# Kernel tuning notes

Measured on AMD Instinct MI355X. Metric: run time of the kernel, lower is better.

Reference implementation:

```python
import jax, jax.numpy as jnp
import numpy as np

B, S, H, C = 16, 4096, 1024, 64

def setup_inputs() -> dict:
    key = jax.random.key(0)
    k1, k2 = jax.random.split(key)
    hidden = jax.random.normal(k1, (B, S, H), dtype=jnp.float32)
    querys = jax.random.normal(k2, (C, H), dtype=jnp.float32)
    return {"hidden": hidden, "querys": querys}

def reference(hidden, querys):
    # scores: [B, C, S] = einsum over hidden_size
    scores = jnp.einsum('bsh,ch->bcs', hidden, querys)
    # softmax over the sequence axis
    factor = jax.nn.softmax(scores, axis=2)
    # pooled: [B, C, H]
    result = jnp.einsum('bcs,bsh->bch', factor, hidden)
    # flatten to [B, C*H]
    return result.reshape(-1, querys.shape[0] * querys.shape[1])
```

## Files before the change

### kernel.cpp

```cpp
#include <hip/hip_runtime.h>
#include <math.h>

#define BB 16
#define SS 4096
#define HH 1024
#define CC 64

typedef __attribute__((ext_vector_type(4))) float f32x4;
typedef __attribute__((ext_vector_type(8))) short s16x8;

__device__ __forceinline__ ushort f2bf(float x) {
    union { float f; unsigned u; } un; un.f = x;
    unsigned r = (un.u + 0x7FFFu + ((un.u >> 16) & 1u)) >> 16;
    return (ushort)r;
}
__device__ __forceinline__ float bf2f(ushort h) {
    union { unsigned u; float f; } un; un.u = ((unsigned)h) << 16; return un.f;
}

__global__ __launch_bounds__(256) void prep_querys_kernel(
    const float* __restrict__ q, ushort* __restrict__ qhi, ushort* __restrict__ qlo)
{
    const int i4 = blockIdx.x * 256 + threadIdx.x;
    const float4 v = ((const float4*)q)[i4];
    ushort4 h, l;
    h.x = f2bf(v.x); l.x = f2bf(v.x - bf2f(h.x));
    h.y = f2bf(v.y); l.y = f2bf(v.y - bf2f(h.y));
    h.z = f2bf(v.z); l.z = f2bf(v.z - bf2f(h.z));
    h.w = f2bf(v.w); l.w = f2bf(v.w - bf2f(h.w));
    ((ushort4*)qhi)[i4] = h;
    ((ushort4*)qlo)[i4] = l;
}

__global__ __launch_bounds__(256) void scores_kernel(
    const float* __restrict__ hidden, const ushort* __restrict__ qhi,
    const ushort* __restrict__ qlo, float* __restrict__ scores)
{
    __shared__ __align__(16) ushort Ahi[128][40];
    __shared__ __align__(16) ushort Alo[128][40];
    __shared__ __align__(16) ushort Bhi[64][40];
    __shared__ __align__(16) ushort Blo[64][40];

    const int b  = blockIdx.y;
    const int s0 = blockIdx.x * 128;
    const int t  = threadIdx.x;
    const int w    = t >> 6;
    const int lane = t & 63;
    const int col  = lane & 15;
    const int quad = lane >> 4;
    const int lr = t >> 3;
    const int lc = t & 7;

    f32x4 acc[2][4];
#pragma unroll
    for (int i = 0; i < 2; ++i)
#pragma unroll
        for (int j = 0; j < 4; ++j) acc[i][j] = (f32x4){0.f, 0.f, 0.f, 0.f};

    const float* hbase = hidden + ((size_t)b * SS + s0) * HH;

    float4 hv[4];
    ushort4 qh[2], ql[2];
#pragma unroll
    for (int p = 0; p < 4; ++p)
        hv[p] = *(const float4*)&hbase[(size_t)(lr + 32 * p) * HH + lc * 4];
#pragma unroll
    for (int p = 0; p < 2; ++p) {
        qh[p] = ((const ushort4*)qhi)[(lr + 32 * p) * 256 + lc];
        ql[p] = ((const ushort4*)qlo)[(lr + 32 * p) * 256 + lc];
    }

    for (int k0 = 0; k0 < HH; k0 += 32) {
        __syncthreads();
#pragma unroll
        for (int p = 0; p < 4; ++p) {
            const int r = lr + 32 * p;
            ushort4 h, l;
            h.x = f2bf(hv[p].x); l.x = f2bf(hv[p].x - bf2f(h.x));
            h.y = f2bf(hv[p].y); l.y = f2bf(hv[p].y - bf2f(h.y));
            h.z = f2bf(hv[p].z); l.z = f2bf(hv[p].z - bf2f(h.z));
            h.w = f2bf(hv[p].w); l.w = f2bf(hv[p].w - bf2f(h.w));
            *(ushort4*)&Ahi[r][lc * 4] = h;
            *(ushort4*)&Alo[r][lc * 4] = l;
        }
#pragma unroll
        for (int p = 0; p < 2; ++p) {
            *(ushort4*)&Bhi[lr + 32 * p][lc * 4] = qh[p];
            *(ushort4*)&Blo[lr + 32 * p][lc * 4] = ql[p];
        }
        __syncthreads();

        if (k0 + 32 < HH) {
            const int kn = k0 + 32;
#pragma unroll
            for (int p = 0; p < 4; ++p)
                hv[p] = *(const float4*)&hbase[(size_t)(lr + 32 * p) * HH + kn + lc * 4];
#pragma unroll
            for (int p = 0; p < 2; ++p) {
                qh[p] = ((const ushort4*)qhi)[(lr + 32 * p) * 256 + kn / 4 + lc];
                ql[p] = ((const ushort4*)qlo)[(lr + 32 * p) * 256 + kn / 4 + lc];
            }
        }

        s16x8 ah[2], al[2], bh[4], bl[4];
#pragma unroll
        for (int mt = 0; mt < 2; ++mt) {
            const int r = w * 32 + mt * 16 + col;
            ah[mt] = *(const s16x8*)&Ahi[r][quad * 8];
            al[mt] = *(const s16x8*)&Alo[r][quad * 8];
        }
#pragma unroll
        for (int nt = 0; nt < 4; ++nt) {
            const int r = nt * 16 + col;
            bh[nt] = *(const s16x8*)&Bhi[r][quad * 8];
            bl[nt] = *(const s16x8*)&Blo[r][quad * 8];
        }
#pragma unroll
        for (int mt = 0; mt < 2; ++mt)
#pragma unroll
            for (int nt = 0; nt < 4; ++nt) {
                acc[mt][nt] = __builtin_amdgcn_mfma_f32_16x16x32_bf16(ah[mt], bh[nt], acc[mt][nt], 0, 0, 0);
                acc[mt][nt] = __builtin_amdgcn_mfma_f32_16x16x32_bf16(ah[mt], bl[nt], acc[mt][nt], 0, 0, 0);
                acc[mt][nt] = __builtin_amdgcn_mfma_f32_16x16x32_bf16(al[mt], bh[nt], acc[mt][nt], 0, 0, 0);
            }
    }

#pragma unroll
    for (int mt = 0; mt < 2; ++mt)
#pragma unroll
        for (int nt = 0; nt < 4; ++nt) {
            const int c = nt * 16 + col;
            const int s = s0 + w * 32 + mt * 16 + quad * 4;
            *(f32x4*)&scores[((size_t)(b * CC + c)) * SS + s] = acc[mt][nt];
        }
}

__global__ __launch_bounds__(256) void softmax_kernel(
    const float* __restrict__ scores, ushort* __restrict__ factor)
{
    const float* p = scores + (size_t)blockIdx.x * SS;
    ushort* f = factor + (size_t)blockIdx.x * SS;
    const int t = threadIdx.x;
    float4 v[4];
    float m = -3.0e38f;
#pragma unroll
    for (int i = 0; i < 4; ++i) {
        v[i] = *(const float4*)&p[t * 4 + i * 1024];
        m = fmaxf(m, fmaxf(fmaxf(v[i].x, v[i].y), fmaxf(v[i].z, v[i].w)));
    }
#pragma unroll
    for (int off = 1; off < 64; off <<= 1) m = fmaxf(m, __shfl_xor(m, off));
    __shared__ float redm[4];
    __shared__ float reds[4];
    const int wave = t >> 6, lane = t & 63;
    if (lane == 0) redm[wave] = m;
    __syncthreads();
    m = fmaxf(fmaxf(redm[0], redm[1]), fmaxf(redm[2], redm[3]));

    float sum = 0.0f;
#pragma unroll
    for (int i = 0; i < 4; ++i) {
        v[i].x = __expf(v[i].x - m); v[i].y = __expf(v[i].y - m);
        v[i].z = __expf(v[i].z - m); v[i].w = __expf(v[i].w - m);
        sum += (v[i].x + v[i].y) + (v[i].z + v[i].w);
    }
#pragma unroll
    for (int off = 1; off < 64; off <<= 1) sum += __shfl_xor(sum, off);
    if (lane == 0) reds[wave] = sum;
    __syncthreads();
    sum = (reds[0] + reds[1]) + (reds[2] + reds[3]);
    const float inv = 1.0f / sum;
#pragma unroll
    for (int i = 0; i < 4; ++i) {
        ushort4 o;
        o.x = f2bf(v[i].x * inv); o.y = f2bf(v[i].y * inv);
        o.z = f2bf(v[i].z * inv); o.w = f2bf(v[i].w * inv);
        ((ushort4*)f)[t + i * 256] = o;
    }
}

__global__ __launch_bounds__(256) void pool_kernel(
    const float* __restrict__ hidden, const ushort* __restrict__ factor,
    float* __restrict__ parts)
{
    __shared__ __align__(16) ushort Ht[64][72];

    const int b  = blockIdx.y;
    const int h0 = blockIdx.x * 64;
    const int ks = blockIdx.z;
    const int sbeg = ks * (SS / 4);
    const int t = threadIdx.x;
    const int w = t >> 6, lane = t & 63, col = lane & 15, quad = lane >> 4;
    const int hc = t & 15;
    const int sq = t >> 4;

    f32x4 acc[4];
#pragma unroll
    for (int j = 0; j < 4; ++j) acc[j] = (f32x4){0.f, 0.f, 0.f, 0.f};

    const float* hbase = hidden + (size_t)b * SS * HH + h0;
    const ushort* fbase = factor + (size_t)(b * CC + w * 16 + col) * SS + sbeg;

    float v[16];
#pragma unroll
    for (int pp = 0; pp < 2; ++pp)
#pragma unroll
        for (int mm = 0; mm < 4; ++mm)
#pragma unroll
            for (int e = 0; e < 2; ++e)
                v[pp * 8 + mm * 2 + e] =
                    hbase[(size_t)(sbeg + 2 * (sq + 16 * pp) + e) * HH + hc + 16 * mm];

    for (int sc = 0; sc < SS / 4; sc += 64) {
        __syncthreads();
#pragma unroll
        for (int pp = 0; pp < 2; ++pp)
#pragma unroll
            for (int mm = 0; mm < 4; ++mm) {
                unsigned pack = (unsigned)f2bf(v[pp * 8 + mm * 2 + 0]) |
                                ((unsigned)f2bf(v[pp * 8 + mm * 2 + 1]) << 16);
                ((unsigned*)Ht)[(hc + 16 * mm) * 36 + (sq + 16 * pp)] = pack;
            }
        __syncthreads();

        const s16x8 fa0 = *(const s16x8*)&fbase[sc + quad * 8];
        const s16x8 fa1 = *(const s16x8*)&fbase[sc + 32 + quad * 8];

        if (sc + 64 < SS / 4) {
#pragma unroll
            for (int pp = 0; pp < 2; ++pp)
#pragma unroll
                for (int mm = 0; mm < 4; ++mm)
#pragma unroll
                    for (int e = 0; e < 2; ++e)
                        v[pp * 8 + mm * 2 + e] =
                            hbase[(size_t)(sbeg + sc + 64 + 2 * (sq + 16 * pp) + e) * HH + hc + 16 * mm];
        }

#pragma unroll
        for (int ksp = 0; ksp < 2; ++ksp) {
            const s16x8 fa = ksp ? fa1 : fa0;
#pragma unroll
            for (int nt = 0; nt < 4; ++nt) {
                const s16x8 hb = *(const s16x8*)&Ht[nt * 16 + col][ksp * 32 + quad * 8];
                acc[nt] = __builtin_amdgcn_mfma_f32_16x16x32_bf16(fa, hb, acc[nt], 0, 0, 0);
            }
        }
    }

    float* dst = parts + (size_t)ks * (BB * CC * HH) + (size_t)b * (CC * HH);
#pragma unroll
    for (int nt = 0; nt < 4; ++nt) {
        const int h = h0 + nt * 16 + col;
#pragma unroll
        for (int r = 0; r < 4; ++r) {
            const int c = w * 16 + quad * 4 + r;
            dst[(size_t)c * HH + h] = acc[nt][r];
        }
    }
}

__global__ __launch_bounds__(256) void reduce4_kernel(
    const float* __restrict__ parts, float* __restrict__ out)
{
    const int i = blockIdx.x * 256 + threadIdx.x;
    const float4* p = (const float4*)parts;
    const float4 a = p[i];
    const float4 b = p[i + 262144];
    const float4 c = p[i + 524288];
    const float4 d = p[i + 786432];
    float4 r;
    r.x = (a.x + b.x) + (c.x + d.x);
    r.y = (a.y + b.y) + (c.y + d.y);
    r.z = (a.z + b.z) + (c.z + d.z);
    r.w = (a.w + b.w) + (c.w + d.w);
    ((float4*)out)[i] = r;
}

extern "C" void kernel_launch(void* const* d_in, const int* in_sizes, int n_in,
                              void* d_out, int out_size, void* d_ws, size_t ws_size,
                              hipStream_t stream)
{
    const float* hidden = (const float*)d_in[0];
    const float* querys = (const float*)d_in[1];
    float* out = (float*)d_out;

    float*  scores = (float*)d_ws;
    float*  parts  = (float*)d_ws;
    ushort* factor = (ushort*)((char*)d_ws + (16u << 20));
    ushort* qhi    = (ushort*)((char*)d_ws + (24u << 20));
    ushort* qlo    = qhi + CC * HH;

    prep_querys_kernel<<<dim3(CC * HH / 1024), 256, 0, stream>>>(querys, qhi, qlo);
    scores_kernel<<<dim3(SS / 128, BB), 256, 0, stream>>>(hidden, qhi, qlo, scores);
    softmax_kernel<<<dim3(BB * CC), 256, 0, stream>>>(scores, factor);
    pool_kernel<<<dim3(HH / 64, BB, 4), 256, 0, stream>>>(hidden, factor, parts);
    reduce4_kernel<<<dim3(1024), 256, 0, stream>>>(parts, out);
}
```

Before: 455.8 us.

## Cache bf16 hidden from scores pass and drop LDS staging in both GEMMs

The scores kernel now loads hidden directly into MFMA register fragments without LDS or barriers, converting with a vectorized hi/lo split. It also writes the bf16-high copy of hidden to workspace. The pool kernel then reads that bf16 copy, half the bytes of fp32, gathering column fragments straight from global memory instead of transposing through LDS. The trade-offs are an extra 128MB write in the scores pass, strided 2-byte gathers in pool, and a rounding mode change (round-half-up rather than round-to-nearest-even).

```diff
diff --git a/kernel.cpp b/kernel.cpp
--- a/kernel.cpp
+++ b/kernel.cpp
@@ -8,6 +8,7 @@
 
 typedef __attribute__((ext_vector_type(4))) float f32x4;
 typedef __attribute__((ext_vector_type(8))) short s16x8;
+typedef __attribute__((ext_vector_type(4))) unsigned int u32x4;
 
 __device__ __forceinline__ ushort f2bf(float x) {
     union { float f; unsigned u; } un; un.f = x;
@@ -16,6 +17,27 @@
 }
 __device__ __forceinline__ float bf2f(ushort h) {
     union { unsigned u; float f; } un; un.u = ((unsigned)h) << 16; return un.f;
+}
+
+__device__ __forceinline__ unsigned hipack(unsigned v1, unsigned v0) {
+    return __builtin_amdgcn_perm(v1, v0, 0x07060302u);
+}
+
+__device__ __forceinline__ void cvt8(f32x4 f0, f32x4 f1, s16x8& hi, s16x8& lo) {
+    u32x4 u0 = __builtin_bit_cast(u32x4, f0);
+    u32x4 u1 = __builtin_bit_cast(u32x4, f1);
+    u32x4 b0 = u0 + 0x8000u;
+    u32x4 b1 = u1 + 0x8000u;
+    f32x4 m0 = __builtin_bit_cast(f32x4, b0 & 0xFFFF0000u);
+    f32x4 m1 = __builtin_bit_cast(f32x4, b1 & 0xFFFF0000u);
+    u32x4 r0 = __builtin_bit_cast(u32x4, f0 - m0);
+    u32x4 r1 = __builtin_bit_cast(u32x4, f1 - m1);
+    u32x4 h = { hipack(b0.y, b0.x), hipack(b0.w, b0.z),
+                hipack(b1.y, b1.x), hipack(b1.w, b1.z) };
+    u32x4 l = { hipack(r0.y, r0.x), hipack(r0.w, r0.z),
+                hipack(r1.y, r1.x), hipack(r1.w, r1.z) };
+    hi = __builtin_bit_cast(s16x8, h);
+    lo = __builtin_bit_cast(s16x8, l);
 }
 
 __global__ __launch_bounds__(256) void prep_querys_kernel(
@@ -34,22 +56,22 @@
 
 __global__ __launch_bounds__(256) void scores_kernel(
     const float* __restrict__ hidden, const ushort* __restrict__ qhi,
-    const ushort* __restrict__ qlo, float* __restrict__ scores)
-{
-    __shared__ __align__(16) ushort Ahi[128][40];
-    __shared__ __align__(16) ushort Alo[128][40];
-    __shared__ __align__(16) ushort Bhi[64][40];
-    __shared__ __align__(16) ushort Blo[64][40];
-
+    const ushort* __restrict__ qlo, float* __restrict__ scores,
+    ushort* __restrict__ hid_hi)
+{
     const int b  = blockIdx.y;
     const int s0 = blockIdx.x * 128;
     const int t  = threadIdx.x;
-    const int w    = t >> 6;
-    const int lane = t & 63;
-    const int col  = lane & 15;
-    const int quad = lane >> 4;
-    const int lr = t >> 3;
-    const int lc = t & 7;
+    const int w = t >> 6, lane = t & 63, col = lane & 15, quad = lane >> 4;
+
+    const int r0 = s0 + w * 32 + col;
+    const int r1 = r0 + 16;
+    const float* a0p = hidden + ((size_t)b * SS + r0) * HH + quad * 8;
+    const float* a1p = hidden + ((size_t)b * SS + r1) * HH + quad * 8;
+    ushort* h0p = hid_hi + ((size_t)b * SS + r0) * HH + quad * 8;
+    ushort* h1p = hid_hi + ((size_t)b * SS + r1) * HH + quad * 8;
+    const ushort* qbh = qhi + (size_t)col * HH + quad * 8;
+    const ushort* qbl = qlo + (size_t)col * HH + quad * 8;
 
     f32x4 acc[2][4];
 #pragma unroll
@@ -57,73 +79,39 @@
 #pragma unroll
         for (int j = 0; j < 4; ++j) acc[i][j] = (f32x4){0.f, 0.f, 0.f, 0.f};
 
-    const float* hbase = hidden + ((size_t)b * SS + s0) * HH;
-
-    float4 hv[4];
-    ushort4 qh[2], ql[2];
-#pragma unroll
-    for (int p = 0; p < 4; ++p)
-        hv[p] = *(const float4*)&hbase[(size_t)(lr + 32 * p) * HH + lc * 4];
-#pragma unroll
-    for (int p = 0; p < 2; ++p) {
-        qh[p] = ((const ushort4*)qhi)[(lr + 32 * p) * 256 + lc];
-        ql[p] = ((const ushort4*)qlo)[(lr + 32 * p) * 256 + lc];
-    }
-
-    for (int k0 = 0; k0 < HH; k0 += 32) {
-        __syncthreads();
-#pragma unroll
-        for (int p = 0; p < 4; ++p) {
-            const int r = lr + 32 * p;
-            ushort4 h, l;
-            h.x = f2bf(hv[p].x); l.x = f2bf(hv[p].x - bf2f(h.x));
-            h.y = f2bf(hv[p].y); l.y = f2bf(hv[p].y - bf2f(h.y));
-            h.z = f2bf(hv[p].z); l.z = f2bf(hv[p].z - bf2f(h.z));
-            h.w = f2bf(hv[p].w); l.w = f2bf(hv[p].w - bf2f(h.w));
-            *(ushort4*)&Ahi[r][lc * 4] = h;
-            *(ushort4*)&Alo[r][lc * 4] = l;
-        }
-#pragma unroll
-        for (int p = 0; p < 2; ++p) {
-            *(ushort4*)&Bhi[lr + 32 * p][lc * 4] = qh[p];
-            *(ushort4*)&Blo[lr + 32 * p][lc * 4] = ql[p];
-        }
-        __syncthreads();
-
-        if (k0 + 32 < HH) {
-            const int kn = k0 + 32;
-#pragma unroll
-            for (int p = 0; p < 4; ++p)
-                hv[p] = *(const float4*)&hbase[(size_t)(lr + 32 * p) * HH + kn + lc * 4];
-#pragma unroll
-            for (int p = 0; p < 2; ++p) {
-                qh[p] = ((const ushort4*)qhi)[(lr + 32 * p) * 256 + kn / 4 + lc];
-                ql[p] = ((const ushort4*)qlo)[(lr + 32 * p) * 256 + kn / 4 + lc];
-            }
-        }
-
-        s16x8 ah[2], al[2], bh[4], bl[4];
-#pragma unroll
-        for (int mt = 0; mt < 2; ++mt) {
-            const int r = w * 32 + mt * 16 + col;
-            ah[mt] = *(const s16x8*)&Ahi[r][quad * 8];
-            al[mt] = *(const s16x8*)&Alo[r][quad * 8];
-        }
-#pragma unroll
-        for (int nt = 0; nt < 4; ++nt) {
-            const int r = nt * 16 + col;
-            bh[nt] = *(const s16x8*)&Bhi[r][quad * 8];
-            bl[nt] = *(const s16x8*)&Blo[r][quad * 8];
-        }
-#pragma unroll
-        for (int mt = 0; mt < 2; ++mt)
-#pragma unroll
-            for (int nt = 0; nt < 4; ++nt) {
-                acc[mt][nt] = __builtin_amdgcn_mfma_f32_16x16x32_bf16(ah[mt], bh[nt], acc[mt][nt], 0, 0, 0);
-                acc[mt][nt] = __builtin_amdgcn_mfma_f32_16x16x32_bf16(ah[mt], bl[nt], acc[mt][nt], 0, 0, 0);
-                acc[mt][nt] = __builtin_amdgcn_mfma_f32_16x16x32_bf16(al[mt], bh[nt], acc[mt][nt], 0, 0, 0);
-            }
-    }
+    f32x4 Aa0, Aa1, Aa2, Aa3, Ab0, Ab1, Ab2, Ab3;
+
+#define LOADA(P0, P1, P2, P3, K) do { \
+    P0 = *(const f32x4*)(a0p + (K));     P1 = *(const f32x4*)(a0p + (K) + 4); \
+    P2 = *(const f32x4*)(a1p + (K));     P3 = *(const f32x4*)(a1p + (K) + 4); } while (0)
+
+#define SCOMP(P0, P1, P2, P3, K) do { \
+    s16x8 ah0, al0, ah1, al1; \
+    cvt8(P0, P1, ah0, al0); \
+    cvt8(P2, P3, ah1, al1); \
+    *(s16x8*)(h0p + (K)) = ah0; \
+    *(s16x8*)(h1p + (K)) = ah1; \
+    _Pragma("unroll") \
+    for (int nt = 0; nt < 4; ++nt) { \
+        const s16x8 bh = *(const s16x8*)(qbh + nt * 16 * HH + (K)); \
+        const s16x8 bl = *(const s16x8*)(qbl + nt * 16 * HH + (K)); \
+        acc[0][nt] = __builtin_amdgcn_mfma_f32_16x16x32_bf16(ah0, bh, acc[0][nt], 0, 0, 0); \
+        acc[0][nt] = __builtin_amdgcn_mfma_f32_16x16x32_bf16(ah0, bl, acc[0][nt], 0, 0, 0); \
+        acc[0][nt] = __builtin_amdgcn_mfma_f32_16x16x32_bf16(al0, bh, acc[0][nt], 0, 0, 0); \
+        acc[1][nt] = __builtin_amdgcn_mfma_f32_16x16x32_bf16(ah1, bh, acc[1][nt], 0, 0, 0); \
+        acc[1][nt] = __builtin_amdgcn_mfma_f32_16x16x32_bf16(ah1, bl, acc[1][nt], 0, 0, 0); \
+        acc[1][nt] = __builtin_amdgcn_mfma_f32_16x16x32_bf16(al1, bh, acc[1][nt], 0, 0, 0); \
+    } } while (0)
+
+    LOADA(Aa0, Aa1, Aa2, Aa3, 0);
+    for (int k0 = 0; k0 < HH; k0 += 64) {
+        LOADA(Ab0, Ab1, Ab2, Ab3, k0 + 32);
+        SCOMP(Aa0, Aa1, Aa2, Aa3, k0);
+        if (k0 + 64 < HH) LOADA(Aa0, Aa1, Aa2, Aa3, k0 + 64);
+        SCOMP(Ab0, Ab1, Ab2, Ab3, k0 + 32);
+    }
+#undef LOADA
+#undef SCOMP
 
 #pragma unroll
     for (int mt = 0; mt < 2; ++mt)
@@ -180,73 +168,51 @@
 }
 
 __global__ __launch_bounds__(256) void pool_kernel(
-    const float* __restrict__ hidden, const ushort* __restrict__ factor,
+    const ushort* __restrict__ hid_hi, const ushort* __restrict__ factor,
     float* __restrict__ parts)
 {
-    __shared__ __align__(16) ushort Ht[64][72];
-
     const int b  = blockIdx.y;
     const int h0 = blockIdx.x * 64;
     const int ks = blockIdx.z;
     const int sbeg = ks * (SS / 4);
     const int t = threadIdx.x;
     const int w = t >> 6, lane = t & 63, col = lane & 15, quad = lane >> 4;
-    const int hc = t & 15;
-    const int sq = t >> 4;
 
     f32x4 acc[4];
 #pragma unroll
     for (int j = 0; j < 4; ++j) acc[j] = (f32x4){0.f, 0.f, 0.f, 0.f};
 
-    const float* hbase = hidden + (size_t)b * SS * HH + h0;
-    const ushort* fbase = factor + (size_t)(b * CC + w * 16 + col) * SS + sbeg;
-
-    float v[16];
-#pragma unroll
-    for (int pp = 0; pp < 2; ++pp)
-#pragma unroll
-        for (int mm = 0; mm < 4; ++mm)
-#pragma unroll
-            for (int e = 0; e < 2; ++e)
-                v[pp * 8 + mm * 2 + e] =
-                    hbase[(size_t)(sbeg + 2 * (sq + 16 * pp) + e) * HH + hc + 16 * mm];
-
+    const ushort* fptr = factor + ((size_t)(b * CC + w * 16 + col)) * SS + sbeg + quad * 8;
+    const ushort* hp = hid_hi + ((size_t)b * SS + sbeg + quad * 8) * HH + h0 + col;
+
+    ushort ra[4][8], rb[4][8];
+    s16x8 faA, faB;
+
+#define PLOAD(R, FA, SC) do { \
+    FA = *(const s16x8*)(fptr + (SC)); \
+    _Pragma("unroll") for (int nt = 0; nt < 4; ++nt) \
+    _Pragma("unroll") for (int j = 0; j < 8; ++j) \
+        R[nt][j] = hp[(size_t)((SC) + j) * HH + nt * 16]; } while (0)
+
+#define PCOMP(R, FA) do { \
+    _Pragma("unroll") for (int nt = 0; nt < 4; ++nt) { \
+        u32x4 d = { (unsigned)R[nt][0] | ((unsigned)R[nt][1] << 16), \
+                    (unsigned)R[nt][2] | ((unsigned)R[nt][3] << 16), \
+                    (unsigned)R[nt][4] | ((unsigned)R[nt][5] << 16), \
+                    (unsigned)R[nt][6] | ((unsigned)R[nt][7] << 16) }; \
+        const s16x8 hb = __builtin_bit_cast(s16x8, d); \
+        acc[nt] = __builtin_amdgcn_mfma_f32_16x16x32_bf16(FA, hb, acc[nt], 0, 0, 0); \
+    } } while (0)
+
+    PLOAD(ra, faA, 0);
     for (int sc = 0; sc < SS / 4; sc += 64) {
-        __syncthreads();
-#pragma unroll
-        for (int pp = 0; pp < 2; ++pp)
-#pragma unroll
-            for (int mm = 0; mm < 4; ++mm) {
-                unsigned pack = (unsigned)f2bf(v[pp * 8 + mm * 2 + 0]) |
-                                ((unsigned)f2bf(v[pp * 8 + mm * 2 + 1]) << 16);
-                ((unsigned*)Ht)[(hc + 16 * mm) * 36 + (sq + 16 * pp)] = pack;
-            }
-        __syncthreads();
-
-        const s16x8 fa0 = *(const s16x8*)&fbase[sc + quad * 8];
-        const s16x8 fa1 = *(const s16x8*)&fbase[sc + 32 + quad * 8];
-
-        if (sc + 64 < SS / 4) {
-#pragma unroll
-            for (int pp = 0; pp < 2; ++pp)
-#pragma unroll
-                for (int mm = 0; mm < 4; ++mm)
-#pragma unroll
-                    for (int e = 0; e < 2; ++e)
-                        v[pp * 8 + mm * 2 + e] =
-                            hbase[(size_t)(sbeg + sc + 64 + 2 * (sq + 16 * pp) + e) * HH + hc + 16 * mm];
-        }
-
-#pragma unroll
-        for (int ksp = 0; ksp < 2; ++ksp) {
-            const s16x8 fa = ksp ? fa1 : fa0;
-#pragma unroll
-            for (int nt = 0; nt < 4; ++nt) {
-                const s16x8 hb = *(const s16x8*)&Ht[nt * 16 + col][ksp * 32 + quad * 8];
-                acc[nt] = __builtin_amdgcn_mfma_f32_16x16x32_bf16(fa, hb, acc[nt], 0, 0, 0);
-            }
-        }
-    }
+        PLOAD(rb, faB, sc + 32);
+        PCOMP(ra, faA);
+        if (sc + 64 < SS / 4) PLOAD(ra, faA, sc + 64);
+        PCOMP(rb, faB);
+    }
+#undef PLOAD
+#undef PCOMP
 
     float* dst = parts + (size_t)ks * (BB * CC * HH) + (size_t)b * (CC * HH);
 #pragma unroll
@@ -290,10 +256,11 @@
     ushort* factor = (ushort*)((char*)d_ws + (16u << 20));
     ushort* qhi    = (ushort*)((char*)d_ws + (24u << 20));
     ushort* qlo    = qhi + CC * HH;
+    ushort* hid_hi = (ushort*)((char*)d_ws + (32u << 20));
 
     prep_querys_kernel<<<dim3(CC * HH / 1024), 256, 0, stream>>>(querys, qhi, qlo);
-    scores_kernel<<<dim3(SS / 128, BB), 256, 0, stream>>>(hidden, qhi, qlo, scores);
+    scores_kernel<<<dim3(SS / 128, BB), 256, 0, stream>>>(hidden, qhi, qlo, scores, hid_hi);
     softmax_kernel<<<dim3(BB * CC), 256, 0, stream>>>(scores, factor);
-    pool_kernel<<<dim3(HH / 64, BB, 4), 256, 0, stream>>>(hidden, factor, parts);
+    pool_kernel<<<dim3(HH / 64, BB, 4), 256, 0, stream>>>(hid_hi, factor, parts);
     reduce4_kernel<<<dim3(1024), 256, 0, stream>>>(parts, out);
 }
```

New measurement: 526.2 us. 15.5% more time.
